# Kernel tuning notes

Hardware: AMD Instinct MI355X
Metric: run time of the kernel (lower is better)

Reference implementation:

```python
import jax, jax.numpy as jnp
import numpy as np

B, N, H = 16, 1024, 768
NEG_INF = -9e15
SLOPE = 0.2


def setup_inputs() -> dict:
    key = jax.random.key(0)
    k1, k2, k3, k4, k5 = jax.random.split(key, 5)
    x = jax.random.normal(k1, (B, N, H), dtype=jnp.float32)
    # node_length acts as a per-node validity mask (float, used via outer product)
    lengths = jax.random.randint(k2, (B,), N // 2, N)
    node_length = (jnp.arange(N)[None, :] < lengths[:, None]).astype(jnp.float32)
    # sparse-ish binary adjacency with self-loops
    adj = (jax.random.uniform(k3, (B, N, N)) < 0.05).astype(jnp.float32)
    adj = jnp.maximum(adj, jnp.eye(N, dtype=jnp.float32)[None])
    # params: kaiming-normal init
    W = jax.random.normal(k4, (H, H), dtype=jnp.float32) * np.sqrt(2.0 / H)
    a = jax.random.normal(k5, (2 * H, 1), dtype=jnp.float32) * np.sqrt(2.0 / (2 * H))
    return {"input": x, "node_length": node_length, "graph_structure": adj, "W": W, "a": a}


def reference(input, node_length, graph_structure, W, a):
    # node_vec = A @ X  [B,N,H]
    node_vec = jnp.matmul(graph_structure, input)
    h = jnp.matmul(node_vec, W)  # [B,N,F]
    F_ = W.shape[1]
    a1 = a[:F_, 0]   # weights on h_i
    a2 = a[F_:, 0]   # weights on h_j
    # e[b,i,j] = leaky_relu(h_i . a1 + h_j . a2)  (identical to concat+matmul with a)
    s1 = jnp.einsum("bnf,f->bn", h, a1)
    s2 = jnp.einsum("bnf,f->bn", h, a2)
    e = jax.nn.leaky_relu(s1[:, :, None] + s2[:, None, :], negative_slope=SLOPE)
    # bias = outer product of node_length; mask where adj or bias <= 1e-6
    bias = node_length[:, :, None] * node_length[:, None, :]
    valid = (graph_structure > 1e-6) & (bias > 1e-6)
    scores = jnp.where(valid, e, NEG_INF)
    attn = jax.nn.softmax(scores, axis=-1)  # attn_dropout=0 -> identity
    return node_vec, attn
```

## Files before the change

### kernel.cpp

```cpp
#include <hip/hip_runtime.h>
#include <hip/hip_bf16.h>

#define BB 16
#define NN 1024
#define HH 768
#define NEG_INF_ -9.0e15f
#define SLOPE_ 0.2f

typedef __bf16 bh8 __attribute__((ext_vector_type(8)));
typedef __bf16 bh4 __attribute__((ext_vector_type(4)));
typedef float f4 __attribute__((ext_vector_type(4)));
typedef unsigned int u32;
typedef unsigned long long u64;


__device__ __forceinline__ float wave_sum0(float v) {
    #pragma unroll
    for (int off = 32; off > 0; off >>= 1) v += __shfl_down(v, off, 64);
    return v;
}
__device__ __forceinline__ float wave_sum_all(float v) {
    #pragma unroll
    for (int off = 1; off < 64; off <<= 1) v += __shfl_xor(v, off, 64);
    return v;
}
__device__ __forceinline__ float wave_max_all(float v) {
    #pragma unroll
    for (int off = 1; off < 64; off <<= 1) v = fmaxf(v, __shfl_xor(v, off, 64));
    return v;
}


__device__ __forceinline__ void gl_lds16(const void* g, void* l) {
    __builtin_amdgcn_global_load_lds(
        (const __attribute__((address_space(1))) u32*)g,
        (__attribute__((address_space(3))) u32*)l, 16, 0, 0);
}


__global__ __launch_bounds__(256) void prep_xt_kernel(const float* __restrict__ adj,
                                                      const float* __restrict__ W,
                                                      const float* __restrict__ a,
                                                      const float* __restrict__ x,
                                                      u64* __restrict__ bits,
                                                      __bf16* __restrict__ xT,
                                                      float* __restrict__ wa1,
                                                      float* __restrict__ wa2,
                                                      float* __restrict__ s1,
                                                      float* __restrict__ s2) {
    __shared__ __bf16 T[32][36];
    const int bid = blockIdx.x;
    const int tid = threadIdx.x;
    const int wave = tid >> 6, lane = tid & 63;

    if (bid < 4096) {
        const int gid = bid * 256 + tid;
        if (gid < BB * NN) { s1[gid] = 0.f; s2[gid] = 0.f; }

        const int row = bid * 4 + wave;
        const float* ar = adj + (size_t)row * NN;
        const int seg = lane >> 4;
        const int sh = (lane & 15) * 4;
        #pragma unroll
        for (int i = 0; i < 4; i++) {
            const int j = lane * 4 + i * 256;
            const float4 av = *(const float4*)(ar + j);
            u32 nib = (av.x > 1e-6f ? 1u : 0u) | (av.y > 1e-6f ? 2u : 0u)
                    | (av.z > 1e-6f ? 4u : 0u) | (av.w > 1e-6f ? 8u : 0u);
            u64 word = (u64)nib << sh;
            word |= __shfl_xor(word, 8, 16);
            word |= __shfl_xor(word, 4, 16);
            word |= __shfl_xor(word, 2, 16);
            word |= __shfl_xor(word, 1, 16);
            if ((lane & 15) == 0) bits[(size_t)row * 16 + i * 4 + seg] = word;
        }

        if (bid < 192) {
            const int f = bid * 4 + wave;
            const float* Wr = W + (size_t)f * HH;
            float v1 = 0.f, v2 = 0.f;
            #pragma unroll
            for (int i = 0; i < 3; i++) {
                const int h = lane * 4 + i * 256;
                const float4 w  = *(const float4*)(Wr + h);
                const float4 a1 = *(const float4*)(a + h);
                const float4 a2 = *(const float4*)(a + HH + h);
                v1 += w.x * a1.x + w.y * a1.y + w.z * a1.z + w.w * a1.w;
                v2 += w.x * a2.x + w.y * a2.y + w.z * a2.z + w.w * a2.w;
            }
            v1 = wave_sum0(v1);
            v2 = wave_sum0(v2);
            if (lane == 0) { wa1[f] = v1; wa2[f] = v2; }
        }
    } else {
        const int u = bid - 4096;
        const int ht = u % 24;
        const int nt = (u / 24) & 31;
        const int b  = u / (24 * 32);
        const int r = tid >> 3;
        const int c = (tid & 7) * 4;
        const float4 v = *(const float4*)(x + ((size_t)b * NN + nt * 32 + r) * HH + ht * 32 + c);
        T[r][c + 0] = (__bf16)v.x; T[r][c + 1] = (__bf16)v.y;
        T[r][c + 2] = (__bf16)v.z; T[r][c + 3] = (__bf16)v.w;

        __syncthreads();
        const int h = tid >> 3;
        const int nc = (tid & 7) * 4;
        bh4 o = { T[nc + 0][h], T[nc + 1][h], T[nc + 2][h], T[nc + 3][h] };
        *(bh4*)(xT + ((size_t)b * HH + ht * 32 + h) * NN + nt * 32 + nc) = o;
    }
}


__global__ __launch_bounds__(256) void gemm_bits(const u64* __restrict__ bits,
                                                 const __bf16* __restrict__ xT,
                                                 const float* __restrict__ wa1,
                                                 const float* __restrict__ wa2,
                                                 float* __restrict__ out,
                                                 float* __restrict__ s1,
                                                 float* __restrict__ s2) {
    __shared__ __bf16 LUT[256 * 8];
    __shared__ __bf16 Bs[2][128 * 64];

    const int orig = blockIdx.x;
    const int g  = (orig >> 6) * 8 + (orig & 7);
    const int bm = (orig >> 3) & 7;
    const int b  = g / 6;
    const int bn = g % 6;

    const int tid = threadIdx.x, lane = tid & 63, wave = tid >> 6;
    const int wr = (wave >> 1) << 6;
    const int wc = (wave & 1) << 6;
    const int quad = lane >> 4, l16 = lane & 15;

    {
        bh8 e;
        #pragma unroll
        for (int j = 0; j < 8; j++) e[j] = ((tid >> j) & 1) ? (__bf16)1.0f : (__bf16)0.0f;
        *(bh8*)&LUT[tid * 8] = e;
    }

    const __bf16* Xb = xT + ((size_t)b * HH + bn * 128) * NN;
    const u64* bgA = bits + ((size_t)b * NN + bm * 128) * 16;

    f4 acc[4][4];
    #pragma unroll
    for (int i = 0; i < 4; i++)
        #pragma unroll
        for (int j = 0; j < 4; j++)
            acc[i][j] = (f4){0.f, 0.f, 0.f, 0.f};

    u64 awc[4];
    #pragma unroll
    for (int i = 0; i < 4; i++)
        awc[i] = bgA[(size_t)(wr + i * 16 + l16) * 16 + 0];

    #pragma unroll
    for (int it = 0; it < 4; it++) {
        const int c = tid + 256 * it;
        const int r = c >> 3, j = c & 7, kc = j ^ (r & 7);
        gl_lds16(Xb + (size_t)r * NN + kc * 8, &Bs[0][r * 64 + j * 8]);
    }
    __syncthreads();

    for (int w = 0; w < 16; ++w) {
        const int cur = w & 1;
        u64 awn[4];
        if (w < 15) {
            const int kt = (w + 1) << 6;
            #pragma unroll
            for (int it = 0; it < 4; it++) {
                const int c = tid + 256 * it;
                const int r = c >> 3, j = c & 7, kc = j ^ (r & 7);
                gl_lds16(Xb + (size_t)r * NN + kt + kc * 8, &Bs[cur ^ 1][r * 64 + j * 8]);
            }
            #pragma unroll
            for (int i = 0; i < 4; i++)
                awn[i] = bgA[(size_t)(wr + i * 16 + l16) * 16 + w + 1];
        }

        #pragma unroll
        for (int s = 0; s < 2; s++) {
            bh8 af[4], bf_[4];
            #pragma unroll
            for (int i = 0; i < 4; i++) {
                const u32 byte = (u32)(awc[i] >> ((s * 4 + quad) * 8)) & 0xffu;
                af[i] = *(const bh8*)&LUT[byte * 8];
            }
            #pragma unroll
            for (int j = 0; j < 4; j++) {
                const int row = wc + j * 16 + l16;
                const int jj = (s * 4 + quad) ^ (row & 7);
                bf_[j] = *(const bh8*)&Bs[cur][row * 64 + jj * 8];
            }
            #pragma unroll
            for (int i = 0; i < 4; i++)
                #pragma unroll
                for (int j = 0; j < 4; j++)
                    acc[i][j] = __builtin_amdgcn_mfma_f32_16x16x32_bf16(af[i], bf_[j], acc[i][j], 0, 0, 0);
        }
        __syncthreads();
        if (w < 15) {
            #pragma unroll
            for (int i = 0; i < 4; i++) awc[i] = awn[i];
        }
    }

    float* Cb = out + (size_t)b * NN * HH + (size_t)bm * 128 * HH + bn * 128;
    const int rbase = wr + quad * 4;
    const int cbase = wc + l16;
    #pragma unroll
    for (int i = 0; i < 4; i++)
        #pragma unroll
        for (int j = 0; j < 4; j++)
            #pragma unroll
            for (int r = 0; r < 4; r++)
                Cb[(size_t)(rbase + i * 16 + r) * HH + cbase + j * 16] = acc[i][j][r];

    float w1j[4], w2j[4];
    #pragma unroll
    for (int j = 0; j < 4; j++) {
        w1j[j] = wa1[bn * 128 + cbase + j * 16];
        w2j[j] = wa2[bn * 128 + cbase + j * 16];
    }
    #pragma unroll
    for (int i = 0; i < 4; i++)
        #pragma unroll
        for (int r = 0; r < 4; r++) {
            float p1 = acc[i][0][r] * w1j[0] + acc[i][1][r] * w1j[1]
                     + acc[i][2][r] * w1j[2] + acc[i][3][r] * w1j[3];
            float p2 = acc[i][0][r] * w2j[0] + acc[i][1][r] * w2j[1]
                     + acc[i][2][r] * w2j[2] + acc[i][3][r] * w2j[3];
            p1 += __shfl_down(p1, 8, 16); p1 += __shfl_down(p1, 4, 16);
            p1 += __shfl_down(p1, 2, 16); p1 += __shfl_down(p1, 1, 16);
            p2 += __shfl_down(p2, 8, 16); p2 += __shfl_down(p2, 4, 16);
            p2 += __shfl_down(p2, 2, 16); p2 += __shfl_down(p2, 1, 16);
            if (l16 == 0) {
                const int n = b * NN + bm * 128 + rbase + i * 16 + r;
                atomicAdd(&s1[n], p1);
                atomicAdd(&s2[n], p2);
            }
        }
}


__global__ __launch_bounds__(256) void softmax_kernel(const u64* __restrict__ bits,
                                                      const float* __restrict__ nl,
                                                      const float* __restrict__ s1,
                                                      const float* __restrict__ s2,
                                                      float* __restrict__ attn) {
    const int row = blockIdx.x * 4 + (threadIdx.x >> 6);
    const int lane = threadIdx.x & 63;
    const int b = row >> 10, n = row & (NN - 1);
    const u64* bwr = bits + (size_t)row * 16;
    const float* nlb = nl + (size_t)b * NN;
    const float* s2b = s2 + (size_t)b * NN;
    const float s1v = s1[row];
    const bool rowok = nlb[n] > 1e-6f;
    const int bitbase = (lane & 15) * 4;

    f4 sc[4];
    float mx = NEG_INF_;
    #pragma unroll
    for (int i = 0; i < 4; i++) {
        const int j = lane * 4 + i * 256;
        const float4 sv = *(const float4*)(s2b + j);
        const float4 nv = *(const float4*)(nlb + j);
        const u64 w64 = bwr[i * 4 + (lane >> 4)];
        const float zs[4] = { s1v + sv.x, s1v + sv.y, s1v + sv.z, s1v + sv.w };
        const float ns[4] = { nv.x, nv.y, nv.z, nv.w };
        #pragma unroll
        for (int e = 0; e < 4; e++) {
            const float z = zs[e];
            const float lr = z > 0.f ? z : SLOPE_ * z;
            const bool valid = rowok && ((w64 >> (bitbase + e)) & 1ull) && (ns[e] > 1e-6f);
            sc[i][e] = valid ? lr : NEG_INF_;
            mx = fmaxf(mx, sc[i][e]);
        }
    }
    mx = wave_max_all(mx);

    f4 ex[4];
    float sum = 0.f;
    #pragma unroll
    for (int i = 0; i < 4; i++)
        #pragma unroll
        for (int e = 0; e < 4; e++) {
            ex[i][e] = __expf(sc[i][e] - mx);
            sum += ex[i][e];
        }
    sum = wave_sum_all(sum);
    const float inv = 1.0f / sum;

    float* outr = attn + (size_t)row * NN;
    #pragma unroll
    for (int i = 0; i < 4; i++) {
        const int j = lane * 4 + i * 256;
        float4 o;
        o.x = ex[i][0] * inv; o.y = ex[i][1] * inv;
        o.z = ex[i][2] * inv; o.w = ex[i][3] * inv;
        *(float4*)(outr + j) = o;
    }
}


extern "C" void kernel_launch(void* const* d_in, const int* in_sizes, int n_in,
                              void* d_out, int out_size, void* d_ws, size_t ws_size,
                              hipStream_t stream) {
    const float* x   = (const float*)d_in[0];
    const float* nl  = (const float*)d_in[1];
    const float* adj = (const float*)d_in[2];
    const float* W   = (const float*)d_in[3];
    const float* a   = (const float*)d_in[4];

    float* out = (float*)d_out;
    float* node_vec = out;
    float* attn = out + (size_t)BB * NN * HH;

    char* wsb = (char*)d_ws;
    float* wa1 = (float*)(wsb);
    float* wa2 = wa1 + HH;
    float* s1  = wa2 + HH;
    float* s2  = s1 + BB * NN;
    u64*    bits = (u64*)(wsb + (1u << 20));
    __bf16* xT   = (__bf16*)(wsb + (4u << 20));

    hipLaunchKernelGGL(prep_xt_kernel, dim3(4096 + 24 * 32 * BB), dim3(256), 0, stream,
                       adj, W, a, x, bits, xT, wa1, wa2, s1, s2);
    hipLaunchKernelGGL(gemm_bits, dim3(768), dim3(256), 0, stream,
                       bits, xT, wa1, wa2, node_vec, s1, s2);
    hipLaunchKernelGGL(softmax_kernel, dim3(4096), dim3(256), 0, stream, bits, nl, s1, s2, attn);
}
```

Baseline: 283.6 us.

## Stage adjacency bits in LDS and deepen X tile prefetch with vmcnt waits

Loads the block's 128x16 packed adjacency bitmask into padded shared memory once, so per-iteration global loads of bit words are no longer needed. It restructures the B-tile double buffer to keep two tiles in flight, issuing the load for tile w+2 after the compute on tile w. Explicit s_waitcnt vmcnt and raw barriers replace __syncthreads so that only the oldest loads are waited on. This adds LDS usage (about 17 KB), which may reduce occupancy, and relies on hand-written counter waits being correct.

```diff
diff --git a/kernel.cpp b/kernel.cpp
--- a/kernel.cpp
+++ b/kernel.cpp
@@ -112,6 +112,8 @@
 }
 
 
+#define BW 17
+
 __global__ __launch_bounds__(256) void gemm_bits(const u64* __restrict__ bits,
                                                  const __bf16* __restrict__ xT,
                                                  const float* __restrict__ wa1,
@@ -120,6 +122,7 @@
                                                  float* __restrict__ s1,
                                                  float* __restrict__ s2) {
     __shared__ __bf16 LUT[256 * 8];
+    __shared__ u64 bitsL[128 * BW];
     __shared__ __bf16 Bs[2][128 * 64];
 
     const int orig = blockIdx.x;
@@ -139,52 +142,55 @@
         for (int j = 0; j < 8; j++) e[j] = ((tid >> j) & 1) ? (__bf16)1.0f : (__bf16)0.0f;
         *(bh8*)&LUT[tid * 8] = e;
     }
+    {
+        const u64* bg = bits + ((size_t)b * NN + bm * 128) * 16;
+        #pragma unroll
+        for (int q = 0; q < 8; q++) {
+            const int gw = tid * 8 + q;
+            bitsL[(gw >> 4) * BW + (gw & 15)] = bg[gw];
+        }
+    }
 
     const __bf16* Xb = xT + ((size_t)b * HH + bn * 128) * NN;
-    const u64* bgA = bits + ((size_t)b * NN + bm * 128) * 16;
-
-    f4 acc[4][4];
-    #pragma unroll
-    for (int i = 0; i < 4; i++)
-        #pragma unroll
-        for (int j = 0; j < 4; j++)
-            acc[i][j] = (f4){0.f, 0.f, 0.f, 0.f};
-
-    u64 awc[4];
-    #pragma unroll
-    for (int i = 0; i < 4; i++)
-        awc[i] = bgA[(size_t)(wr + i * 16 + l16) * 16 + 0];
-
+
+    const __bf16* sSrc[4]; int sOff[4];
     #pragma unroll
     for (int it = 0; it < 4; it++) {
         const int c = tid + 256 * it;
         const int r = c >> 3, j = c & 7, kc = j ^ (r & 7);
-        gl_lds16(Xb + (size_t)r * NN + kc * 8, &Bs[0][r * 64 + j * 8]);
-    }
-    __syncthreads();
+        sSrc[it] = Xb + (size_t)r * NN + kc * 8;
+        sOff[it] = c * 8;
+    }
+
+    f4 acc[4][4];
+    #pragma unroll
+    for (int i = 0; i < 4; i++)
+        #pragma unroll
+        for (int j = 0; j < 4; j++)
+            acc[i][j] = (f4){0.f, 0.f, 0.f, 0.f};
+
+    #pragma unroll
+    for (int it = 0; it < 4; it++) gl_lds16(sSrc[it] + 0,  &Bs[0][sOff[it]]);
+    #pragma unroll
+    for (int it = 0; it < 4; it++) gl_lds16(sSrc[it] + 64, &Bs[1][sOff[it]]);
+    asm volatile("s_waitcnt lgkmcnt(0) vmcnt(4)" ::: "memory");
+    __builtin_amdgcn_s_barrier();
+    asm volatile("" ::: "memory");
 
     for (int w = 0; w < 16; ++w) {
         const int cur = w & 1;
-        u64 awn[4];
-        if (w < 15) {
-            const int kt = (w + 1) << 6;
-            #pragma unroll
-            for (int it = 0; it < 4; it++) {
-                const int c = tid + 256 * it;
-                const int r = c >> 3, j = c & 7, kc = j ^ (r & 7);
-                gl_lds16(Xb + (size_t)r * NN + kt + kc * 8, &Bs[cur ^ 1][r * 64 + j * 8]);
-            }
-            #pragma unroll
-            for (int i = 0; i < 4; i++)
-                awn[i] = bgA[(size_t)(wr + i * 16 + l16) * 16 + w + 1];
-        }
+
+        u64 aw[4];
+        #pragma unroll
+        for (int i = 0; i < 4; i++)
+            aw[i] = bitsL[(wr + i * 16 + l16) * BW + w];
 
         #pragma unroll
         for (int s = 0; s < 2; s++) {
             bh8 af[4], bf_[4];
             #pragma unroll
             for (int i = 0; i < 4; i++) {
-                const u32 byte = (u32)(awc[i] >> ((s * 4 + quad) * 8)) & 0xffu;
+                const u32 byte = (u32)(aw[i] >> ((s * 4 + quad) * 8)) & 0xffu;
                 af[i] = *(const bh8*)&LUT[byte * 8];
             }
             #pragma unroll
@@ -199,10 +205,20 @@
                 for (int j = 0; j < 4; j++)
                     acc[i][j] = __builtin_amdgcn_mfma_f32_16x16x32_bf16(af[i], bf_[j], acc[i][j], 0, 0, 0);
         }
-        __syncthreads();
-        if (w < 15) {
-            #pragma unroll
-            for (int i = 0; i < 4; i++) awc[i] = awn[i];
+
+        if (w < 14) {
+            __builtin_amdgcn_s_barrier();
+            asm volatile("" ::: "memory");
+            const int kt = (w + 2) << 6;
+            #pragma unroll
+            for (int it = 0; it < 4; it++) gl_lds16(sSrc[it] + kt, &Bs[cur][sOff[it]]);
+            asm volatile("s_waitcnt vmcnt(4)" ::: "memory");
+            __builtin_amdgcn_s_barrier();
+            asm volatile("" ::: "memory");
+        } else if (w == 14) {
+            asm volatile("s_waitcnt vmcnt(0)" ::: "memory");
+            __builtin_amdgcn_s_barrier();
+            asm volatile("" ::: "memory");
         }
     }
 
```

After: 266.0 us. -6.2%, faster.
